# Kernel optimization log

Measured on AMD Instinct MI355X. Metric: run time of the kernel, lower is better.

Reference implementation:

```python
import jax, jax.numpy as jnp
import numpy as np

# Brevitas-style binary quant constants:
# SignedBinaryWeightPerTensorConst -> sign(w) * 0.1 (const per-tensor scale)
# SignedBinaryActPerTensorConst    -> sign(x) * 1.0
W_SCALE = 0.1
A_SCALE = 1.0
EMBED = 9984  # 128 channels * 78 spatial


def _sign(x):
    return jnp.where(x >= 0, 1.0, -1.0).astype(x.dtype)


def bin_w(w):
    # binary weight quant with straight-through estimator
    q = W_SCALE * _sign(w)
    return w + jax.lax.stop_gradient(q - w)


def bin_act(x):
    # QuantHardTanh with binary act quant: forward = sign(x)*A_SCALE,
    # backward = hardtanh gradient (clip to [-1, 1])
    ht = jnp.clip(x, -1.0, 1.0)
    q = A_SCALE * _sign(x)
    return ht + jax.lax.stop_gradient(q - ht)


def scale_bias(x, s, b):
    # QuantScaleBias: per-channel scale (binary-quantized) + bias
    sq = bin_w(s)
    if x.ndim == 3:  # (N, C, L)
        return x * sq[None, :, None] + b[None, :, None]
    return x * sq[None, :] + b[None, :]


def conv1d(x, w, dilation):
    return jax.lax.conv_general_dilated(
        x, w, window_strides=(1,), padding='VALID',
        rhs_dilation=(dilation,), dimension_numbers=('NCH', 'OIH', 'NCH'))


def maxpool1d(x, k):
    return jax.lax.reduce_window(x, -jnp.inf, jax.lax.max,
                                 (1, 1, k), (1, 1, k), 'VALID')


def forward(x, s0, b0, w1, s1, b1, w2, s2, b2, w3, s3, b3,
            w4, s4, b4, w5, s5, b5, fw1, s6, b6, fw2, s7, b7):
    x = scale_bias(x, s0, b0)                     # (N,3,16000)
    x = conv1d(x, bin_w(w1), 1)                   # (N,64,15960)
    x = bin_act(scale_bias(x, s1, b1))
    x = maxpool1d(x, 3)                           # (N,64,5320)
    x = conv1d(x, bin_w(w2), 2)                   # (N,64,5240)
    x = bin_act(scale_bias(x, s2, b2))
    x = maxpool1d(x, 3)                           # (N,64,1746)
    x = conv1d(x, bin_w(w3), 2)                   # (N,128,1666)
    x = bin_act(scale_bias(x, s3, b3))
    x = maxpool1d(x, 3)                           # (N,128,555)
    x = conv1d(x, bin_w(w4), 2)                   # (N,128,475)
    x = bin_act(scale_bias(x, s4, b4))
    x = maxpool1d(x, 3)                           # (N,128,158)
    x = conv1d(x, bin_w(w5), 2)                   # (N,128,78)
    x = bin_act(scale_bias(x, s5, b5))
    x = x.reshape(-1, EMBED)                      # (N,9984)
    x = x @ bin_w(fw1).T                          # (N,1024)
    x = bin_act(scale_bias(x, s6, b6))
    x = x @ bin_w(fw2).T                          # (N,1000)
    x = scale_bias(x, s7, b7)
    return x


def setup_inputs() -> dict:
    key = jax.random.key(0)
    ks = jax.random.split(key, 24)
    n = lambda k, shp: jax.random.normal(k, shp, dtype=jnp.float32) * 0.05
    return {
        'x': jax.random.normal(ks[0], (64, 3, 16000), dtype=jnp.float32),
        's0': n(ks[1], (3,)), 'b0': n(ks[2], (3,)),
        'w1': n(ks[3], (64, 3, 41)), 's1': n(ks[4], (64,)), 'b1': n(ks[5], (64,)),
        'w2': n(ks[6], (64, 64, 41)), 's2': n(ks[7], (64,)), 'b2': n(ks[8], (64,)),
        'w3': n(ks[9], (128, 64, 41)), 's3': n(ks[10], (128,)), 'b3': n(ks[11], (128,)),
        'w4': n(ks[12], (128, 128, 41)), 's4': n(ks[13], (128,)), 'b4': n(ks[14], (128,)),
        'w5': n(ks[15], (128, 128, 41)), 's5': n(ks[16], (128,)), 'b5': n(ks[17], (128,)),
        'fw1': n(ks[18], (1024, EMBED)), 's6': n(ks[19], (1024,)), 'b6': n(ks[20], (1024,)),
        'fw2': n(ks[21], (1000, 1024)), 's7': n(ks[22], (1000,)), 'b7': n(ks[23], (1000,)),
    }


def reference(x, s0, b0, w1, s1, b1, w2, s2, b2, w3, s3, b3,
              w4, s4, b4, w5, s5, b5, fw1, s6, b6, fw2, s7, b7):
    return forward(x, s0, b0, w1, s1, b1, w2, s2, b2, w3, s3, b3,
                   w4, s4, b4, w5, s5, b5, fw1, s6, b6, fw2, s7, b7)
```

## Files before the change

### kernel.cpp

```cpp
#include <hip/hip_runtime.h>
#include <cstdint>

typedef unsigned long long u64;
typedef unsigned int u32;

#define L_X 16000
#define NB  64
#define P1  5320
#define P2  1746
#define P3  555
#define P4  158
#define C5  78

__device__ __forceinline__ void chain64(float& A, u64 u) {
    u32 w = (u32)u;
    #pragma unroll
    for (int j = 0; j < 32; ++j)
        A = __fadd_rn(A, __uint_as_float(0x3DCCCCCDu | ((w << (31 - j)) & 0x80000000u)));
    w = (u32)(u >> 32);
    #pragma unroll
    for (int j = 0; j < 32; ++j)
        A = __fadd_rn(A, __uint_as_float(0x3DCCCCCDu | ((w << (31 - j)) & 0x80000000u)));
}

__global__ void pack_w1k(const float* __restrict__ w1, u64* __restrict__ dst) {
    int t = blockIdx.x * blockDim.x + threadIdx.x;
    if (t >= 41 * 3) return;
    int ci = t % 3;
    int k = t / 3;
    u64 word = 0;
    for (int co = 0; co < 64; ++co)
        if (w1[(co * 3 + ci) * 41 + k] < 0.f) word |= 1ull << co;
    dst[k * 4 + ci] = word;
}

__global__ void pack_wT(const float* __restrict__ w, u64* __restrict__ wT,
                        int Co, int CIW) {
    int t = blockIdx.x * blockDim.x + threadIdx.x;
    if (t >= Co * 41 * CIW) return;
    int co = t % Co;
    int rem = t / Co;
    int h = rem % CIW;
    int k = rem / CIW;
    int CI = CIW * 64;
    u64 word = 0;
    for (int c = 0; c < 64; ++c)
        if (w[((size_t)co * CI + h * 64 + c) * 41 + k] < 0.f) word |= 1ull << c;
    wT[t] = word;
}

__global__ void pack_fw1T(const float* __restrict__ w, u64* __restrict__ wT) {
    int t = blockIdx.x * blockDim.x + threadIdx.x;
    if (t >= 156 * 1024) return;
    int row = t & 1023;
    int j = t >> 10;
    const float* base = w + (size_t)row * 9984 + j * 64;
    u64 word = 0;
    for (int c = 0; c < 64; ++c)
        if (base[c] < 0.f) word |= 1ull << c;
    wT[t] = word;
}

__global__ void pack_fw2T(const float* __restrict__ w, u64* __restrict__ wT) {
    int t = blockIdx.x * blockDim.x + threadIdx.x;
    if (t >= 16 * 1000) return;
    int row = t % 1000;
    int j = t / 1000;
    const float* base = w + (size_t)row * 1024 + j * 64;
    u64 word = 0;
    for (int c = 0; c < 64; ++c)
        if (base[c] < 0.f) word |= 1ull << c;
    wT[t] = word;
}

__global__ void repack_a5(const u64* __restrict__ a5, u64* __restrict__ a5F) {
    int t = blockIdx.x * blockDim.x + threadIdx.x;
    if (t >= NB * 156) return;
    int j = t % 156;
    int n = t / 156;
    u64 word = 0;
    #pragma unroll
    for (int c = 0; c < 64; ++c) {
        int jj = j * 64 + c;
        int chan = jj / 78;
        int tp = jj - chan * 78;
        u64 src = a5[((size_t)n * C5 + tp) * 2 + (chan >> 6)];
        word |= ((src >> (chan & 63)) & 1ull) << c;
    }
    a5F[t] = word;
}

__global__ __launch_bounds__(64) void conv1_s(
        const float* __restrict__ x, const u64* __restrict__ w1k,
        const float* __restrict__ s0, const float* __restrict__ b0,
        const float* __restrict__ s1, const float* __restrict__ b1,
        u64* __restrict__ a1) {
    __shared__ float yl[3][232];
    __shared__ float s1l[64], b1l[64];
    int lane = threadIdx.x;
    int qb = blockIdx.x * 64;
    int n = blockIdx.y;

    #pragma unroll
    for (int ci = 0; ci < 3; ++ci) {
        float sq = (s0[ci] < 0.f) ? -0.1f : 0.1f;
        float bb = b0[ci];
        const float* xp = x + ((size_t)n * 3 + ci) * L_X;
        for (int i = lane; i < 232; i += 64) {
            int t = 3 * qb + i;
            t = (t < L_X) ? t : (L_X - 1);
            float xsb = __fadd_rn(__fmul_rn(xp[t], sq), bb);
            yl[ci][i] = __fmul_rn(xsb, 0.1f);
        }
    }
    s1l[lane] = s1[lane];
    b1l[lane] = b1[lane];
    __syncthreads();

    int q = qb + lane;
    bool valid = q < P1;
    int base = 3 * lane;
    u64 word = 0;

    #pragma unroll 1
    for (int tile = 0; tile < 4; ++tile) {
        float S[16][3];
        #pragma unroll
        for (int c = 0; c < 16; ++c)
            #pragma unroll
            for (int r = 0; r < 3; ++r) S[c][r] = 0.f;

        #pragma unroll 1
        for (int k = 0; k < 41; ++k) {
            float y0[3], y1[3], y2[3];
            #pragma unroll
            for (int r = 0; r < 3; ++r) {
                y0[r] = yl[0][base + k + r];
                y1[r] = yl[1][base + k + r];
                y2[r] = yl[2][base + k + r];
            }
            u32 t0 = (u32)(w1k[k * 4 + 0] >> (tile * 16));
            u32 t1 = (u32)(w1k[k * 4 + 1] >> (tile * 16));
            u32 t2 = (u32)(w1k[k * 4 + 2] >> (tile * 16));
            #pragma unroll
            for (int c = 0; c < 16; ++c) {
                float wf0 = __uint_as_float(0x3F800000u | (((t0 >> c) & 1u) << 31));
                float wf1 = __uint_as_float(0x3F800000u | (((t1 >> c) & 1u) << 31));
                float wf2 = __uint_as_float(0x3F800000u | (((t2 >> c) & 1u) << 31));
                #pragma unroll
                for (int r = 0; r < 3; ++r) {
                    float A = __fmul_rn(y0[r], wf0);
                    A = __fmaf_rn(y1[r], wf1, A);
                    A = __fmaf_rn(y2[r], wf2, A);
                    S[c][r] = __fadd_rn(S[c][r], A);
                }
            }
        }
        #pragma unroll
        for (int c = 0; c < 16; ++c) {
            int co = tile * 16 + c;
            float sq1 = (s1l[co] < 0.f) ? -0.1f : 0.1f;
            float bb1 = b1l[co];
            bool neg = true;
            #pragma unroll
            for (int r = 0; r < 3; ++r) {
                float pre = __fadd_rn(__fmul_rn(S[c][r], sq1), bb1);
                neg = neg && (pre < 0.f);
            }
            word |= (u64)(neg ? 1 : 0) << co;
        }
    }
    if (valid) a1[(size_t)n * P1 + q] = word;
}

template <int CIW, int POOLK>
__global__ void bconv_g(const u64* __restrict__ abits_in, const u64* __restrict__ wT,
                        const float* __restrict__ s, const float* __restrict__ b,
                        u64* __restrict__ abits_out, int Lin, int Lq, double G) {
    constexpr int BITS = 41 * CIW * 64;
    int q = blockIdx.x;
    int n = blockIdx.y;
    int co = threadIdx.x;
    int Co = blockDim.x;
    int wave = co >> 6;
    int CoW = Co >> 6;
    float sqf = (s[co] < 0.f) ? -0.1f : 0.1f;
    float bf  = b[co];
    const u64* wp = wT + co;
    const u64* ap = abits_in + ((size_t)n * Lin + (size_t)POOLK * q) * CIW;

    int pc[POOLK];
    #pragma unroll
    for (int r = 0; r < POOLK; ++r) pc[r] = 0;
    #pragma unroll 1
    for (int k = 0; k < 41; ++k) {
        u64 wk[CIW];
        #pragma unroll
        for (int h = 0; h < CIW; ++h) wk[h] = wp[((size_t)k * CIW + h) * Co];
        const u64* ak = ap + (size_t)(2 * k) * CIW;
        #pragma unroll
        for (int r = 0; r < POOLK; ++r) {
            #pragma unroll
            for (int h = 0; h < CIW; ++h)
                pc[r] += (int)__popcll(ak[r * CIW + h] ^ wk[h]);
        }
    }
    const double vv = (double)0.1f * (double)0.1f;
    double svv = (sqf < 0.f) ? -vv : vv;
    double bd = (double)bf;
    bool negr[POOLK];
    bool flagr[POOLK];
    #pragma unroll
    for (int r = 0; r < POOLK; ++r) {
        double pre = (double)(BITS - 2 * pc[r]) * svv + bd;
        negr[r] = (pre < 0.0);
        flagr[r] = (fabs(pre) < G);
    }
    #pragma unroll
    for (int r = 0; r < POOLK; ++r) {
        if (__ballot(flagr[r]) != 0ull) {
            float S = 0.f;
            #pragma unroll 1
            for (int k = 0; k < 41; ++k) {
                float A = 0.f;
                #pragma unroll
                for (int h = 0; h < CIW; ++h) {
                    u64 u = ap[(size_t)(2 * k + r) * CIW + h]
                          ^ wp[((size_t)k * CIW + h) * Co];
                    chain64(A, u);
                }
                S = __fadd_rn(S, A);
            }
            negr[r] = (__fadd_rn(__fmul_rn(S, sqf), bf) < 0.f);
        }
    }
    bool neg = true;
    #pragma unroll
    for (int r = 0; r < POOLK; ++r) neg = neg && negr[r];
    u64 word = __ballot(neg);
    if ((co & 63) == 0) abits_out[((size_t)n * Lq + q) * CoW + wave] = word;
}

__global__ __launch_bounds__(64) void fc1_k(
        const u64* __restrict__ a5F, const u64* __restrict__ fw1T,
        const float* __restrict__ s6, const float* __restrict__ b6,
        u64* __restrict__ y6b) {
    int g = blockIdx.x;
    int n = blockIdx.y;
    int lane = threadIdx.x;
    int row = g * 64 + lane;
    float S = 0.f;
    #pragma unroll 1
    for (int j = 0; j < 156; ++j) {
        u64 u = a5F[(size_t)n * 156 + j] ^ fw1T[(size_t)j * 1024 + row];
        chain64(S, u);
    }
    float pre = __fadd_rn(__fmul_rn(S, (s6[row] < 0.f) ? -0.1f : 0.1f), b6[row]);
    u64 word = __ballot(pre < 0.f);
    if (lane == 0) y6b[n * 16 + g] = word;
}

__global__ void fc2_k(const u64* __restrict__ y6b, const u64* __restrict__ fw2T,
                      const float* __restrict__ s7, const float* __restrict__ b7,
                      float* __restrict__ out) {
    int t = blockIdx.x * blockDim.x + threadIdx.x;
    if (t >= NB * 1000) return;
    int r = t % 1000;
    int n = t / 1000;
    float S = 0.f;
    #pragma unroll 1
    for (int j = 0; j < 16; ++j) {
        u64 u = y6b[n * 16 + j] ^ fw2T[j * 1000 + r];
        chain64(S, u);
    }
    out[t] = __fadd_rn(__fmul_rn(S, (s7[r] < 0.f) ? -0.1f : 0.1f), b7[r]);
}

extern "C" void kernel_launch(void* const* d_in, const int* in_sizes, int n_in,
                              void* d_out, int out_size, void* d_ws, size_t ws_size,
                              hipStream_t stream) {
    const float* x   = (const float*)d_in[0];
    const float* s0  = (const float*)d_in[1];
    const float* b0  = (const float*)d_in[2];
    const float* w1  = (const float*)d_in[3];
    const float* s1  = (const float*)d_in[4];
    const float* b1  = (const float*)d_in[5];
    const float* w2  = (const float*)d_in[6];
    const float* s2  = (const float*)d_in[7];
    const float* b2  = (const float*)d_in[8];
    const float* w3  = (const float*)d_in[9];
    const float* s3  = (const float*)d_in[10];
    const float* b3  = (const float*)d_in[11];
    const float* w4  = (const float*)d_in[12];
    const float* s4  = (const float*)d_in[13];
    const float* b4  = (const float*)d_in[14];
    const float* w5  = (const float*)d_in[15];
    const float* s5  = (const float*)d_in[16];
    const float* b5  = (const float*)d_in[17];
    const float* fw1 = (const float*)d_in[18];
    const float* s6  = (const float*)d_in[19];
    const float* b6  = (const float*)d_in[20];
    const float* fw2 = (const float*)d_in[21];
    const float* s7  = (const float*)d_in[22];
    const float* b7  = (const float*)d_in[23];

    u64* p = (u64*)d_ws;
    u64* w1kb = p; p += 41 * 4;
    u64* w2T  = p; p += 41 * 64;
    u64* w3T  = p; p += 41 * 128;
    u64* w4T  = p; p += 82 * 128;
    u64* w5T  = p; p += 82 * 128;
    u64* fw1T = p; p += 156 * 1024;
    u64* fw2T = p; p += 16 * 1000;
    u64* a1   = p; p += (size_t)NB * P1;
    u64* a2   = p; p += (size_t)NB * P2;
    u64* a3   = p; p += (size_t)NB * P3 * 2;
    u64* a4   = p; p += (size_t)NB * P4 * 2;
    u64* a5   = p; p += (size_t)NB * C5 * 2;
    u64* a5F  = p; p += (size_t)NB * 156;
    u64* y6b  = p; p += (size_t)NB * 16;

    const double G64  = 2.0e-4;
    const double G128 = 5.0e-4;

    pack_w1k<<<1, 128, 0, stream>>>(w1, w1kb);
    pack_wT<<<(64 * 41 + 255) / 256, 256, 0, stream>>>(w2, w2T, 64, 1);
    pack_wT<<<(128 * 41 + 255) / 256, 256, 0, stream>>>(w3, w3T, 128, 1);
    pack_wT<<<(128 * 82 + 255) / 256, 256, 0, stream>>>(w4, w4T, 128, 2);
    pack_wT<<<(128 * 82 + 255) / 256, 256, 0, stream>>>(w5, w5T, 128, 2);
    pack_fw1T<<<(156 * 1024 + 255) / 256, 256, 0, stream>>>(fw1, fw1T);
    pack_fw2T<<<(16 * 1000 + 255) / 256, 256, 0, stream>>>(fw2, fw2T);

    conv1_s<<<dim3((P1 + 63) / 64, NB), 64, 0, stream>>>(x, w1kb, s0, b0, s1, b1, a1);
    bconv_g<1, 3><<<dim3(P2, NB), 64, 0, stream>>>(a1, w2T, s2, b2, a2, P1, P2, G64);
    bconv_g<1, 3><<<dim3(P3, NB), 128, 0, stream>>>(a2, w3T, s3, b3, a3, P2, P3, G64);
    bconv_g<2, 3><<<dim3(P4, NB), 128, 0, stream>>>(a3, w4T, s4, b4, a4, P3, P4, G128);
    bconv_g<2, 1><<<dim3(C5, NB), 128, 0, stream>>>(a4, w5T, s5, b5, a5, P4, C5, G128);
    repack_a5<<<(NB * 156 + 255) / 256, 256, 0, stream>>>(a5, a5F);
    fc1_k<<<dim3(16, NB), 64, 0, stream>>>(a5F, fw1T, s6, b6, y6b);
    fc2_k<<<(NB * 1000 + 255) / 256, 256, 0, stream>>>(y6b, fw2T, s7, b7, (float*)d_out);
}
```

Before: 1.107 ms.

## Split conv1 channels across grid z and tile four outputs per bconv block

conv1 now uses 128-thread blocks and a third grid dimension that splits the 64 output channels into two 32-channel halves. Each half writes a u32 word, which doubles the number of blocks and halves per-thread serial work. The conv1 weight words are also prefetched one tap ahead. The binary conv kernels now handle four pooled outputs per block, reusing each weight load across them and cutting the block count by four. The cost is more registers per thread and duplicated input staging in conv1.

New measurement: 1.573 ms. +42.0%, slower.

```diff
diff --git a/kernel.cpp b/kernel.cpp
--- a/kernel.cpp
+++ b/kernel.cpp
@@ -90,48 +90,59 @@
     a5F[t] = word;
 }
 
-__global__ __launch_bounds__(64) void conv1_s(
+__global__ __launch_bounds__(128) void conv1_s(
         const float* __restrict__ x, const u64* __restrict__ w1k,
         const float* __restrict__ s0, const float* __restrict__ b0,
         const float* __restrict__ s1, const float* __restrict__ b1,
-        u64* __restrict__ a1) {
-    __shared__ float yl[3][232];
-    __shared__ float s1l[64], b1l[64];
-    int lane = threadIdx.x;
-    int qb = blockIdx.x * 64;
+        u32* __restrict__ a1w) {
+    __shared__ float yl[3][424];
+    __shared__ float s1l[32], b1l[32];
+    int tid = threadIdx.x;
+    int qb = blockIdx.x * 128;
     int n = blockIdx.y;
+    int z = blockIdx.z;
 
     #pragma unroll
     for (int ci = 0; ci < 3; ++ci) {
         float sq = (s0[ci] < 0.f) ? -0.1f : 0.1f;
         float bb = b0[ci];
         const float* xp = x + ((size_t)n * 3 + ci) * L_X;
-        for (int i = lane; i < 232; i += 64) {
+        for (int i = tid; i < 424; i += 128) {
             int t = 3 * qb + i;
             t = (t < L_X) ? t : (L_X - 1);
             float xsb = __fadd_rn(__fmul_rn(xp[t], sq), bb);
             yl[ci][i] = __fmul_rn(xsb, 0.1f);
         }
     }
-    s1l[lane] = s1[lane];
-    b1l[lane] = b1[lane];
+    if (tid < 32) {
+        s1l[tid] = s1[z * 32 + tid];
+        b1l[tid] = b1[z * 32 + tid];
+    }
     __syncthreads();
 
-    int q = qb + lane;
+    int q = qb + tid;
     bool valid = q < P1;
-    int base = 3 * lane;
-    u64 word = 0;
-
-    #pragma unroll 1
-    for (int tile = 0; tile < 4; ++tile) {
+    int base = 3 * tid;
+    u32 word = 0;
+
+    #pragma unroll 1
+    for (int sub = 0; sub < 2; ++sub) {
+        int shift = z * 32 + sub * 16;
         float S[16][3];
         #pragma unroll
         for (int c = 0; c < 16; ++c)
             #pragma unroll
             for (int r = 0; r < 3; ++r) S[c][r] = 0.f;
 
+        u64 m0 = w1k[0 * 4 + 0], m1 = w1k[0 * 4 + 1], m2 = w1k[0 * 4 + 2];
         #pragma unroll 1
         for (int k = 0; k < 41; ++k) {
+            u64 p0 = 0, p1 = 0, p2 = 0;
+            if (k < 40) {
+                p0 = w1k[(k + 1) * 4 + 0];
+                p1 = w1k[(k + 1) * 4 + 1];
+                p2 = w1k[(k + 1) * 4 + 2];
+            }
             float y0[3], y1[3], y2[3];
             #pragma unroll
             for (int r = 0; r < 3; ++r) {
@@ -139,9 +150,9 @@
                 y1[r] = yl[1][base + k + r];
                 y2[r] = yl[2][base + k + r];
             }
-            u32 t0 = (u32)(w1k[k * 4 + 0] >> (tile * 16));
-            u32 t1 = (u32)(w1k[k * 4 + 1] >> (tile * 16));
-            u32 t2 = (u32)(w1k[k * 4 + 2] >> (tile * 16));
+            u32 t0 = (u32)(m0 >> shift);
+            u32 t1 = (u32)(m1 >> shift);
+            u32 t2 = (u32)(m2 >> shift);
             #pragma unroll
             for (int c = 0; c < 16; ++c) {
                 float wf0 = __uint_as_float(0x3F800000u | (((t0 >> c) & 1u) << 31));
@@ -155,30 +166,31 @@
                     S[c][r] = __fadd_rn(S[c][r], A);
                 }
             }
+            m0 = p0; m1 = p1; m2 = p2;
         }
         #pragma unroll
         for (int c = 0; c < 16; ++c) {
-            int co = tile * 16 + c;
-            float sq1 = (s1l[co] < 0.f) ? -0.1f : 0.1f;
-            float bb1 = b1l[co];
+            int cl = sub * 16 + c;
+            float sq1 = (s1l[cl] < 0.f) ? -0.1f : 0.1f;
+            float bb1 = b1l[cl];
             bool neg = true;
             #pragma unroll
             for (int r = 0; r < 3; ++r) {
                 float pre = __fadd_rn(__fmul_rn(S[c][r], sq1), bb1);
                 neg = neg && (pre < 0.f);
             }
-            word |= (u64)(neg ? 1 : 0) << co;
-        }
-    }
-    if (valid) a1[(size_t)n * P1 + q] = word;
-}
-
-template <int CIW, int POOLK>
+            word |= (u32)(neg ? 1 : 0) << cl;
+        }
+    }
+    if (valid) a1w[((size_t)n * P1 + q) * 2 + z] = word;
+}
+
+template <int CIW, int POOLK, int QT>
 __global__ void bconv_g(const u64* __restrict__ abits_in, const u64* __restrict__ wT,
                         const float* __restrict__ s, const float* __restrict__ b,
                         u64* __restrict__ abits_out, int Lin, int Lq, double G) {
     constexpr int BITS = 41 * CIW * 64;
-    int q = blockIdx.x;
+    int qb = blockIdx.x * QT;
     int n = blockIdx.y;
     int co = threadIdx.x;
     int Co = blockDim.x;
@@ -187,58 +199,77 @@
     float sqf = (s[co] < 0.f) ? -0.1f : 0.1f;
     float bf  = b[co];
     const u64* wp = wT + co;
-    const u64* ap = abits_in + ((size_t)n * Lin + (size_t)POOLK * q) * CIW;
-
-    int pc[POOLK];
-    #pragma unroll
-    for (int r = 0; r < POOLK; ++r) pc[r] = 0;
+    const u64* an = abits_in + (size_t)n * Lin * CIW;
+
+    int poff[QT];
+    #pragma unroll
+    for (int i = 0; i < QT; ++i)
+        poff[i] = POOLK * min(qb + i, Lq - 1);
+
+    int pc[QT][POOLK];
+    #pragma unroll
+    for (int i = 0; i < QT; ++i)
+        #pragma unroll
+        for (int r = 0; r < POOLK; ++r) pc[i][r] = 0;
+
     #pragma unroll 1
     for (int k = 0; k < 41; ++k) {
         u64 wk[CIW];
         #pragma unroll
         for (int h = 0; h < CIW; ++h) wk[h] = wp[((size_t)k * CIW + h) * Co];
-        const u64* ak = ap + (size_t)(2 * k) * CIW;
-        #pragma unroll
-        for (int r = 0; r < POOLK; ++r) {
-            #pragma unroll
-            for (int h = 0; h < CIW; ++h)
-                pc[r] += (int)__popcll(ak[r * CIW + h] ^ wk[h]);
-        }
-    }
+        #pragma unroll
+        for (int i = 0; i < QT; ++i)
+            #pragma unroll
+            for (int r = 0; r < POOLK; ++r)
+                #pragma unroll
+                for (int h = 0; h < CIW; ++h)
+                    pc[i][r] += (int)__popcll(an[(size_t)(poff[i] + r + 2 * k) * CIW + h] ^ wk[h]);
+    }
+
     const double vv = (double)0.1f * (double)0.1f;
     double svv = (sqf < 0.f) ? -vv : vv;
     double bd = (double)bf;
-    bool negr[POOLK];
-    bool flagr[POOLK];
-    #pragma unroll
-    for (int r = 0; r < POOLK; ++r) {
-        double pre = (double)(BITS - 2 * pc[r]) * svv + bd;
-        negr[r] = (pre < 0.0);
-        flagr[r] = (fabs(pre) < G);
-    }
-    #pragma unroll
-    for (int r = 0; r < POOLK; ++r) {
-        if (__ballot(flagr[r]) != 0ull) {
-            float S = 0.f;
-            #pragma unroll 1
-            for (int k = 0; k < 41; ++k) {
-                float A = 0.f;
-                #pragma unroll
-                for (int h = 0; h < CIW; ++h) {
-                    u64 u = ap[(size_t)(2 * k + r) * CIW + h]
-                          ^ wp[((size_t)k * CIW + h) * Co];
-                    chain64(A, u);
+    bool negr[QT][POOLK], flagr[QT][POOLK];
+    #pragma unroll
+    for (int i = 0; i < QT; ++i)
+        #pragma unroll
+        for (int r = 0; r < POOLK; ++r) {
+            double pre = (double)(BITS - 2 * pc[i][r]) * svv + bd;
+            negr[i][r] = (pre < 0.0);
+            flagr[i][r] = (fabs(pre) < G);
+        }
+
+    #pragma unroll 1
+    for (int i = 0; i < QT; ++i) {
+        #pragma unroll 1
+        for (int r = 0; r < POOLK; ++r) {
+            if (__ballot(flagr[i][r]) != 0ull) {
+                float S = 0.f;
+                #pragma unroll 1
+                for (int k = 0; k < 41; ++k) {
+                    float A = 0.f;
+                    #pragma unroll
+                    for (int h = 0; h < CIW; ++h) {
+                        u64 u = an[(size_t)(poff[i] + r + 2 * k) * CIW + h]
+                              ^ wp[((size_t)k * CIW + h) * Co];
+                        chain64(A, u);
+                    }
+                    S = __fadd_rn(S, A);
                 }
-                S = __fadd_rn(S, A);
-            }
-            negr[r] = (__fadd_rn(__fmul_rn(S, sqf), bf) < 0.f);
-        }
-    }
-    bool neg = true;
-    #pragma unroll
-    for (int r = 0; r < POOLK; ++r) neg = neg && negr[r];
-    u64 word = __ballot(neg);
-    if ((co & 63) == 0) abits_out[((size_t)n * Lq + q) * CoW + wave] = word;
+                negr[i][r] = (__fadd_rn(__fmul_rn(S, sqf), bf) < 0.f);
+            }
+        }
+    }
+
+    #pragma unroll
+    for (int i = 0; i < QT; ++i) {
+        bool neg = true;
+        #pragma unroll
+        for (int r = 0; r < POOLK; ++r) neg = neg && negr[i][r];
+        u64 word = __ballot(neg);
+        int qi = min(qb + i, Lq - 1);
+        if ((co & 63) == 0) abits_out[((size_t)n * Lq + qi) * CoW + wave] = word;
+    }
 }
 
 __global__ __launch_bounds__(64) void fc1_k(
@@ -331,11 +362,12 @@
     pack_fw1T<<<(156 * 1024 + 255) / 256, 256, 0, stream>>>(fw1, fw1T);
     pack_fw2T<<<(16 * 1000 + 255) / 256, 256, 0, stream>>>(fw2, fw2T);
 
-    conv1_s<<<dim3((P1 + 63) / 64, NB), 64, 0, stream>>>(x, w1kb, s0, b0, s1, b1, a1);
-    bconv_g<1, 3><<<dim3(P2, NB), 64, 0, stream>>>(a1, w2T, s2, b2, a2, P1, P2, G64);
-    bconv_g<1, 3><<<dim3(P3, NB), 128, 0, stream>>>(a2, w3T, s3, b3, a3, P2, P3, G64);
-    bconv_g<2, 3><<<dim3(P4, NB), 128, 0, stream>>>(a3, w4T, s4, b4, a4, P3, P4, G128);
-    bconv_g<2, 1><<<dim3(C5, NB), 128, 0, stream>>>(a4, w5T, s5, b5, a5, P4, C5, G128);
+    conv1_s<<<dim3((P1 + 127) / 128, NB, 2), 128, 0, stream>>>(
+        x, w1kb, s0, b0, s1, b1, (u32*)a1);
+    bconv_g<1, 3, 4><<<dim3((P2 + 3) / 4, NB), 64, 0, stream>>>(a1, w2T, s2, b2, a2, P1, P2, G64);
+    bconv_g<1, 3, 4><<<dim3((P3 + 3) / 4, NB), 128, 0, stream>>>(a2, w3T, s3, b3, a3, P2, P3, G64);
+    bconv_g<2, 3, 4><<<dim3((P4 + 3) / 4, NB), 128, 0, stream>>>(a3, w4T, s4, b4, a4, P3, P4, G128);
+    bconv_g<2, 1, 4><<<dim3((C5 + 3) / 4, NB), 128, 0, stream>>>(a4, w5T, s5, b5, a5, P4, C5, G128);
     repack_a5<<<(NB * 156 + 255) / 256, 256, 0, stream>>>(a5, a5F);
     fc1_k<<<dim3(16, NB), 64, 0, stream>>>(a5F, fw1T, s6, b6, y6b);
     fc2_k<<<(NB * 1000 + 255) / 256, 256, 0, stream>>>(y6b, fw2T, s7, b7, (float*)d_out);
```

## Merge weight-packing kernels and skip exact recompute when pool max is decided

Applied to the files above, without the earlier changes.

Replaces seven separate weight-packing launches with a single segmented pack_all kernel, removing several launch overheads. In the binary conv kernel, the exact float-order recompute for a pooled position is now skipped when another position in the pool window is clearly positive, because the max-pool result is then known without resolving near-zero ties. This cuts the slow chain64 fallback work but adds a bit of per-thread logic. Mixing divergent segments in one pack kernel may slightly unbalance the work.

After: 993.2 us. 10.3% less time.

```diff
diff --git a/kernel.cpp b/kernel.cpp
--- a/kernel.cpp
+++ b/kernel.cpp
@@ -23,21 +23,15 @@
         A = __fadd_rn(A, __uint_as_float(0x3DCCCCCDu | ((w << (31 - j)) & 0x80000000u)));
 }
 
-__global__ void pack_w1k(const float* __restrict__ w1, u64* __restrict__ dst) {
-    int t = blockIdx.x * blockDim.x + threadIdx.x;
-    if (t >= 41 * 3) return;
-    int ci = t % 3;
-    int k = t / 3;
-    u64 word = 0;
-    for (int co = 0; co < 64; ++co)
-        if (w1[(co * 3 + ci) * 41 + k] < 0.f) word |= 1ull << co;
-    dst[k * 4 + ci] = word;
-}
-
-__global__ void pack_wT(const float* __restrict__ w, u64* __restrict__ wT,
-                        int Co, int CIW) {
-    int t = blockIdx.x * blockDim.x + threadIdx.x;
-    if (t >= Co * 41 * CIW) return;
+#define SEG0 123
+#define SEG1 (SEG0 + 2624)
+#define SEG2 (SEG1 + 5248)
+#define SEG3 (SEG2 + 10496)
+#define SEG4 (SEG3 + 10496)
+#define SEG5 (SEG4 + 159744)
+#define SEG6 (SEG5 + 16000)
+
+__device__ __forceinline__ void pack_conv(const float* w, u64* wT, int t, int Co, int CIW) {
     int co = t % Co;
     int rem = t / Co;
     int h = rem % CIW;
@@ -49,28 +43,49 @@
     wT[t] = word;
 }
 
-__global__ void pack_fw1T(const float* __restrict__ w, u64* __restrict__ wT) {
-    int t = blockIdx.x * blockDim.x + threadIdx.x;
-    if (t >= 156 * 1024) return;
-    int row = t & 1023;
-    int j = t >> 10;
-    const float* base = w + (size_t)row * 9984 + j * 64;
-    u64 word = 0;
-    for (int c = 0; c < 64; ++c)
-        if (base[c] < 0.f) word |= 1ull << c;
-    wT[t] = word;
-}
-
-__global__ void pack_fw2T(const float* __restrict__ w, u64* __restrict__ wT) {
-    int t = blockIdx.x * blockDim.x + threadIdx.x;
-    if (t >= 16 * 1000) return;
-    int row = t % 1000;
-    int j = t / 1000;
-    const float* base = w + (size_t)row * 1024 + j * 64;
-    u64 word = 0;
-    for (int c = 0; c < 64; ++c)
-        if (base[c] < 0.f) word |= 1ull << c;
-    wT[t] = word;
+__global__ void pack_all(const float* __restrict__ w1, const float* __restrict__ w2,
+                         const float* __restrict__ w3, const float* __restrict__ w4,
+                         const float* __restrict__ w5, const float* __restrict__ fw1,
+                         const float* __restrict__ fw2,
+                         u64* __restrict__ w1k, u64* __restrict__ w2T,
+                         u64* __restrict__ w3T, u64* __restrict__ w4T,
+                         u64* __restrict__ w5T, u64* __restrict__ fw1T,
+                         u64* __restrict__ fw2T) {
+    int tid = blockIdx.x * blockDim.x + threadIdx.x;
+    if (tid < SEG0) {
+        int ci = tid % 3;
+        int k = tid / 3;
+        u64 word = 0;
+        for (int co = 0; co < 64; ++co)
+            if (w1[(co * 3 + ci) * 41 + k] < 0.f) word |= 1ull << co;
+        w1k[k * 4 + ci] = word;
+    } else if (tid < SEG1) {
+        pack_conv(w2, w2T, tid - SEG0, 64, 1);
+    } else if (tid < SEG2) {
+        pack_conv(w3, w3T, tid - SEG1, 128, 1);
+    } else if (tid < SEG3) {
+        pack_conv(w4, w4T, tid - SEG2, 128, 2);
+    } else if (tid < SEG4) {
+        pack_conv(w5, w5T, tid - SEG3, 128, 2);
+    } else if (tid < SEG5) {
+        int t = tid - SEG4;
+        int row = t & 1023;
+        int j = t >> 10;
+        const float* base = fw1 + (size_t)row * 9984 + j * 64;
+        u64 word = 0;
+        for (int c = 0; c < 64; ++c)
+            if (base[c] < 0.f) word |= 1ull << c;
+        fw1T[t] = word;
+    } else if (tid < SEG6) {
+        int t = tid - SEG5;
+        int row = t % 1000;
+        int j = t / 1000;
+        const float* base = fw2 + (size_t)row * 1024 + j * 64;
+        u64 word = 0;
+        for (int c = 0; c < 64; ++c)
+            if (base[c] < 0.f) word |= 1ull << c;
+        fw2T[t] = word;
+    }
 }
 
 __global__ void repack_a5(const u64* __restrict__ a5, u64* __restrict__ a5F) {
@@ -208,17 +223,22 @@
     const double vv = (double)0.1f * (double)0.1f;
     double svv = (sqf < 0.f) ? -vv : vv;
     double bd = (double)bf;
-    bool negr[POOLK];
-    bool flagr[POOLK];
+    bool negr[POOLK], flagr[POOLK], nn[POOLK];
     #pragma unroll
     for (int r = 0; r < POOLK; ++r) {
         double pre = (double)(BITS - 2 * pc[r]) * svv + bd;
         negr[r] = (pre < 0.0);
         flagr[r] = (fabs(pre) < G);
+        nn[r] = (pre > G);
     }
     #pragma unroll
     for (int r = 0; r < POOLK; ++r) {
-        if (__ballot(flagr[r]) != 0ull) {
+        bool other_nn = false;
+        #pragma unroll
+        for (int r2 = 0; r2 < POOLK; ++r2)
+            if (r2 != r) other_nn = other_nn || nn[r2];
+        bool need = flagr[r] && !other_nn;
+        if (__ballot(need) != 0ull) {
             float S = 0.f;
             #pragma unroll 1
             for (int k = 0; k < 41; ++k) {
@@ -323,13 +343,8 @@
     const double G64  = 2.0e-4;
     const double G128 = 5.0e-4;
 
-    pack_w1k<<<1, 128, 0, stream>>>(w1, w1kb);
-    pack_wT<<<(64 * 41 + 255) / 256, 256, 0, stream>>>(w2, w2T, 64, 1);
-    pack_wT<<<(128 * 41 + 255) / 256, 256, 0, stream>>>(w3, w3T, 128, 1);
-    pack_wT<<<(128 * 82 + 255) / 256, 256, 0, stream>>>(w4, w4T, 128, 2);
-    pack_wT<<<(128 * 82 + 255) / 256, 256, 0, stream>>>(w5, w5T, 128, 2);
-    pack_fw1T<<<(156 * 1024 + 255) / 256, 256, 0, stream>>>(fw1, fw1T);
-    pack_fw2T<<<(16 * 1000 + 255) / 256, 256, 0, stream>>>(fw2, fw2T);
+    pack_all<<<(SEG6 + 255) / 256, 256, 0, stream>>>(
+        w1, w2, w3, w4, w5, fw1, fw2, w1kb, w2T, w3T, w4T, w5T, fw1T, fw2T);
 
     conv1_s<<<dim3((P1 + 63) / 64, NB), 64, 0, stream>>>(x, w1kb, s0, b0, s1, b1, a1);
     bconv_g<1, 3><<<dim3(P2, NB), 64, 0, stream>>>(a1, w2T, s2, b2, a2, P1, P2, G64);
```
